# Performance work log

Measured on AMD Instinct MI355X. Metric: run time of the kernel, lower is better.

## Reference

```python
import jax, jax.numpy as jnp
import numpy as np

L, N, I, H = 512, 512, 128, 128

def setup_inputs() -> dict:
    key = jax.random.key(0)
    ks = jax.random.split(key, 6)
    inp = {
        'input': jax.random.normal(ks[0], (L, N, I), dtype=jnp.float32),
        'hc': jnp.zeros((N, 2 * H), dtype=jnp.float32),
        'is_initial': jax.random.randint(ks[1], (L, N), 0, 2, dtype=jnp.int32),
        'W_ih': jax.random.normal(ks[2], (4 * H, I), dtype=jnp.float32) * (1.0 / np.sqrt(H)),
        'W_hh': jax.random.normal(ks[3], (4 * H, H), dtype=jnp.float32) * (1.0 / np.sqrt(H)),
        'b_ih': jax.random.normal(ks[4], (4 * H,), dtype=jnp.float32) * 0.01,
        'b_hh': jax.random.normal(ks[5], (4 * H,), dtype=jnp.float32) * 0.01,
    }
    return inp

def reference(input, hc, is_initial, W_ih, W_hh, b_ih, b_hh):
    h0, c0 = jnp.split(hc, 2, axis=-1)                 # [N,H] each
    mask = 1.0 - is_initial.astype(input.dtype)        # [L,N]; 0 where episode resets

    def step(carry, xm):
        h, c = carry
        x, m = xm                                      # x:[N,I], m:[N]
        h = h * m[:, None]
        c = c * m[:, None]
        # PyTorch LSTMCell gate order: i, f, g, o
        gates = x @ W_ih.T + b_ih + h @ W_hh.T + b_hh  # [N,4H]
        i_g, f_g, g_g, o_g = jnp.split(gates, 4, axis=-1)
        i_g = jax.nn.sigmoid(i_g)
        f_g = jax.nn.sigmoid(f_g)
        g_g = jnp.tanh(g_g)
        o_g = jax.nn.sigmoid(o_g)
        c = f_g * c + i_g * g_g
        h = o_g * jnp.tanh(c)
        return (h, c), h

    (h, c), outputs = jax.lax.scan(step, (h0, c0), (input, mask))
    # final hc: cat([h,c],-1) is [N,2H]; with N==L the expand(L,-1) is a no-op
    hc_out = jnp.broadcast_to(jnp.concatenate([h, c], axis=-1), (L, 2 * H))
    return outputs, hc_out
```

## Files before the change

kernel.cpp:

```cpp
#include <hip/hip_runtime.h>
#include <hip/hip_fp16.h>
#include <stdint.h>

#define LT 512
#define NB 512
#define DI 128
#define DH 128
#define AROW 272
#define ASTR 34

typedef _Float16 f16;
typedef __attribute__((ext_vector_type(2))) _Float16 f16x2;
typedef __attribute__((ext_vector_type(8))) _Float16 f16x8;
typedef __attribute__((ext_vector_type(4))) float floatx4;

__device__ __forceinline__ uint32_t pack2(float x, float y) {
    f16x2 p;
    p.x = (_Float16)x;
    p.y = (_Float16)y;
    return __builtin_bit_cast(uint32_t, p);
}

__device__ __forceinline__ float frcp(float x) {
#if __has_builtin(__builtin_amdgcn_rcpf)
    return __builtin_amdgcn_rcpf(x);
#else
    return 1.f / x;
#endif
}

__device__ __forceinline__ float sigm(float v) {
    return frcp(1.f + __expf(-v));
}

__device__ __forceinline__ float tanh_(float v) {
    float a = fabsf(v);
    float e = __expf(-2.f * a);
    float r = (1.f - e) * frcp(1.f + e);
    return v < 0.f ? -r : r;
}

__launch_bounds__(512, 2)
__global__ void lstm_fused_mfma(const float* __restrict__ x,
                                const float* __restrict__ hc0,
                                const int*   __restrict__ isini,
                                const float* __restrict__ Wih,
                                const float* __restrict__ Whh,
                                const float* __restrict__ bih,
                                const float* __restrict__ bhh,
                                float* __restrict__ out)
{
    const int tid  = threadIdx.x;
    const int lane = tid & 63;
    const int w    = tid >> 6;
    const int l16  = lane & 15;
    const int quad = lane >> 4;
    const int n0   = blockIdx.x * 2;
    const int j    = w * 16 + l16;

    __shared__ __align__(16) f16 sh_a[2][2][AROW];
    __shared__ float sh_m[2][LT];

    for (int t = tid; t < LT; t += 512) {
        sh_m[0][t] = 1.f - (float)isini[(size_t)t * NB + n0];
        sh_m[1][t] = 1.f - (float)isini[(size_t)t * NB + n0 + 1];
    }

    f16x8 bfrag[4][8];
    float bs[4];
#pragma unroll
    for (int gs = 0; gs < 4; ++gs) {
        const int gate = gs * 128 + j;
        bs[gs] = bih[gate] + bhh[gate];
        const float4* wi = (const float4*)(Wih + (size_t)gate * DI);
        const float4* wh = (const float4*)(Whh + (size_t)gate * DH);
#pragma unroll
        for (int kc = 0; kc < 4; ++kc) {
            float4 a = wi[kc * 8 + quad * 2];
            float4 b = wi[kc * 8 + quad * 2 + 1];
            uint4 u;
            u.x = pack2(a.x, a.y); u.y = pack2(a.z, a.w);
            u.z = pack2(b.x, b.y); u.w = pack2(b.z, b.w);
            bfrag[gs][kc] = __builtin_bit_cast(f16x8, u);
        }
#pragma unroll
        for (int kc = 0; kc < 4; ++kc) {
            float4 a = wh[kc * 8 + quad * 2];
            float4 b = wh[kc * 8 + quad * 2 + 1];
            uint4 u;
            u.x = pack2(a.x, a.y); u.y = pack2(a.z, a.w);
            u.z = pack2(b.x, b.y); u.w = pack2(b.z, b.w);
            bfrag[gs][4 + kc] = __builtin_bit_cast(f16x8, u);
        }
    }

    const bool act = (quad & 1) == 0;
    const int  nr  = quad >> 1;
    const int  n   = n0 + nr;

    float cval = 0.f, hval = 0.f, mcur = 0.f;
    if (act) {
        hval = hc0[(size_t)n * (2 * DH) + j];
        cval = hc0[(size_t)n * (2 * DH) + DH + j];
        mcur = 1.f - (float)isini[n];
        sh_a[0][nr][128 + j] = (f16)(hval * mcur);
    }

    const int  sflat = w * 8 + (lane & 7);
    const int  srow  = sflat >> 5;
    const int  sf4   = sflat & 31;
    const bool sact  = (lane & 63) < 8;
    float4 xp = {0.f, 0.f, 0.f, 0.f};
    if (sact) {
        const float4* sp0 = (const float4*)(x + ((size_t)0 * NB + n0 + srow) * DI);
        float4 v = sp0[sf4];
        uint2 u2;
        u2.x = pack2(v.x, v.y); u2.y = pack2(v.z, v.w);
        *(uint2*)&sh_a[0][srow][sf4 * 4] = u2;
        const float4* sp1 = (const float4*)(x + ((size_t)1 * NB + n0 + srow) * DI);
        xp = sp1[sf4];
    }
    __syncthreads();

    const int rowsel = l16 >> 3;
    float* outp = out + (size_t)n * DH + j;

    for (int t = 0; t < LT; ++t) {
        const int buf  = t & 1;
        const int nbuf = buf ^ 1;

        const uint4* ab = (const uint4*)&sh_a[buf][0][0];
        f16x8 af[8];
#pragma unroll
        for (int kc = 0; kc < 8; ++kc)
            af[kc] = __builtin_bit_cast(f16x8, ab[rowsel * ASTR + kc * 4 + quad]);

        if (sact) {
            uint2 u2;
            u2.x = pack2(xp.x, xp.y); u2.y = pack2(xp.z, xp.w);
            *(uint2*)&sh_a[nbuf][srow][sf4 * 4] = u2;
            int t2 = (t + 2 < LT) ? (t + 2) : (LT - 1);
            const float4* sp = (const float4*)(x + ((size_t)t2 * NB + n0 + srow) * DI);
            xp = sp[sf4];
        }

        floatx4 acc[4];
#pragma unroll
        for (int gs = 0; gs < 4; ++gs) acc[gs] = (floatx4){0.f, 0.f, 0.f, 0.f};
#pragma unroll
        for (int kc = 0; kc < 8; ++kc) {
#pragma unroll
            for (int gs = 0; gs < 4; ++gs)
                acc[gs] = __builtin_amdgcn_mfma_f32_16x16x32_f16(
                    af[kc], bfrag[gs][kc], acc[gs], 0, 0, 0);
        }

        if (act) {
            float ig = acc[0][0] + bs[0];
            float fg = acc[1][0] + bs[1];
            float gg = acc[2][0] + bs[2];
            float og = acc[3][0] + bs[3];
            float cc = sigm(fg) * (mcur * cval) + sigm(ig) * tanh_(gg);
            hval = sigm(og) * tanh_(cc);
            cval = cc;
            outp[(size_t)t * (NB * DH)] = hval;
            int t1 = (t + 1 < LT) ? (t + 1) : (LT - 1);
            float mn = sh_m[nr][t1];
            sh_a[nbuf][nr][128 + j] = (f16)(hval * mn);
            mcur = mn;
        }
        __syncthreads();
    }

    if (act) {
        size_t base = (size_t)LT * NB * DH;
        out[base + (size_t)n * (2 * DH) + j]      = hval;
        out[base + (size_t)n * (2 * DH) + DH + j] = cval;
    }
}

extern "C" void kernel_launch(void* const* d_in, const int* in_sizes, int n_in,
                              void* d_out, int out_size, void* d_ws, size_t ws_size,
                              hipStream_t stream) {
    const float* x     = (const float*)d_in[0];
    const float* hc0   = (const float*)d_in[1];
    const int*   isini = (const int*)d_in[2];
    const float* Wih   = (const float*)d_in[3];
    const float* Whh   = (const float*)d_in[4];
    const float* bih   = (const float*)d_in[5];
    const float* bhh   = (const float*)d_in[6];
    float* out = (float*)d_out;

    lstm_fused_mfma<<<dim3(NB / 2), dim3(512), 0, stream>>>(
        x, hc0, isini, Wih, Whh, bih, bhh, out);
}
```

Measured before the change: 590.5 us.

## Batch input projection every 8 steps into LDS ring, halve recurrent MFMA chain

The input-to-gate projection is taken off the serial per-step critical path. Every 8 timesteps it is computed for 8 future steps at once, using a 16-row MFMA tile over staged x, and stored as packed fp16 in an LDS ring buffer. The per-step recurrent GEMM now only covers the 128-wide hidden state (4 k-chunks instead of 8), and the per-step barrier becomes a raw s_barrier after an lgkmcnt wait. The trade-offs are more LDS use, a periodic burst of extra work every 8 steps, and gate pre-activations rounded to fp16.

```diff
diff --git a/kernel.cpp b/kernel.cpp
--- a/kernel.cpp
+++ b/kernel.cpp
@@ -6,8 +6,6 @@
 #define NB 512
 #define DI 128
 #define DH 128
-#define AROW 272
-#define ASTR 34
 
 typedef _Float16 f16;
 typedef __attribute__((ext_vector_type(2))) _Float16 f16x2;
@@ -41,14 +39,14 @@
 }
 
 __launch_bounds__(512, 2)
-__global__ void lstm_fused_mfma(const float* __restrict__ x,
-                                const float* __restrict__ hc0,
-                                const int*   __restrict__ isini,
-                                const float* __restrict__ Wih,
-                                const float* __restrict__ Whh,
-                                const float* __restrict__ bih,
-                                const float* __restrict__ bhh,
-                                float* __restrict__ out)
+__global__ void lstm_fused_v2(const float* __restrict__ x,
+                              const float* __restrict__ hc0,
+                              const int*   __restrict__ isini,
+                              const float* __restrict__ Wih,
+                              const float* __restrict__ Whh,
+                              const float* __restrict__ bih,
+                              const float* __restrict__ bhh,
+                              float* __restrict__ out)
 {
     const int tid  = threadIdx.x;
     const int lane = tid & 63;
@@ -58,31 +56,22 @@
     const int n0   = blockIdx.x * 2;
     const int j    = w * 16 + l16;
 
-    __shared__ __align__(16) f16 sh_a[2][2][AROW];
+    __shared__ __align__(16) f16   sh_h[2][2][136];
+    __shared__ __align__(16) f16   xs[2][16][136];
+    __shared__ __align__(16) uint2 ring[16][2][128];
     __shared__ float sh_m[2][LT];
 
-    for (int t = tid; t < LT; t += 512) {
-        sh_m[0][t] = 1.f - (float)isini[(size_t)t * NB + n0];
-        sh_m[1][t] = 1.f - (float)isini[(size_t)t * NB + n0 + 1];
-    }
-
-    f16x8 bfrag[4][8];
+    sh_m[0][tid] = 1.f - (float)isini[(size_t)tid * NB + n0];
+    sh_m[1][tid] = 1.f - (float)isini[(size_t)tid * NB + n0 + 1];
+
+    f16x8 bH[4][4], bI[4][4];
     float bs[4];
 #pragma unroll
     for (int gs = 0; gs < 4; ++gs) {
         const int gate = gs * 128 + j;
         bs[gs] = bih[gate] + bhh[gate];
+        const float4* wh = (const float4*)(Whh + (size_t)gate * DH);
         const float4* wi = (const float4*)(Wih + (size_t)gate * DI);
-        const float4* wh = (const float4*)(Whh + (size_t)gate * DH);
-#pragma unroll
-        for (int kc = 0; kc < 4; ++kc) {
-            float4 a = wi[kc * 8 + quad * 2];
-            float4 b = wi[kc * 8 + quad * 2 + 1];
-            uint4 u;
-            u.x = pack2(a.x, a.y); u.y = pack2(a.z, a.w);
-            u.z = pack2(b.x, b.y); u.w = pack2(b.z, b.w);
-            bfrag[gs][kc] = __builtin_bit_cast(f16x8, u);
-        }
 #pragma unroll
         for (int kc = 0; kc < 4; ++kc) {
             float4 a = wh[kc * 8 + quad * 2];
@@ -90,86 +79,156 @@
             uint4 u;
             u.x = pack2(a.x, a.y); u.y = pack2(a.z, a.w);
             u.z = pack2(b.x, b.y); u.w = pack2(b.z, b.w);
-            bfrag[gs][4 + kc] = __builtin_bit_cast(f16x8, u);
-        }
-    }
+            bH[gs][kc] = __builtin_bit_cast(f16x8, u);
+            a = wi[kc * 8 + quad * 2];
+            b = wi[kc * 8 + quad * 2 + 1];
+            u.x = pack2(a.x, a.y); u.y = pack2(a.z, a.w);
+            u.z = pack2(b.x, b.y); u.w = pack2(b.z, b.w);
+            bI[gs][kc] = __builtin_bit_cast(f16x8, u);
+        }
+    }
+
+    {
+        const int m = tid >> 5, f4 = tid & 31;
+        const int d = m >> 1, nrr = m & 1;
+        const float4* sp = (const float4*)(x + ((size_t)d * NB + n0 + nrr) * DI);
+        float4 v = sp[f4];
+        uint2 u2; u2.x = pack2(v.x, v.y); u2.y = pack2(v.z, v.w);
+        *(uint2*)&xs[0][m][f4 * 4] = u2;
+    }
+    __syncthreads();
 
     const bool act = (quad & 1) == 0;
     const int  nr  = quad >> 1;
     const int  n   = n0 + nr;
-
-    float cval = 0.f, hval = 0.f, mcur = 0.f;
+    const int  rowsel = l16 >> 3;
+
+    float hval = 0.f, cval = 0.f, mcur = 0.f;
     if (act) {
         hval = hc0[(size_t)n * (2 * DH) + j];
         cval = hc0[(size_t)n * (2 * DH) + DH + j];
-        mcur = 1.f - (float)isini[n];
-        sh_a[0][nr][128 + j] = (f16)(hval * mcur);
+        mcur = sh_m[nr][0];
+        sh_h[0][nr][j] = (f16)(hval * mcur);
+    }
+
+    {
+        const uint4* xb = (const uint4*)&xs[0][0][0];
+        f16x8 axf[4];
+#pragma unroll
+        for (int kc = 0; kc < 4; ++kc)
+            axf[kc] = __builtin_bit_cast(f16x8, xb[l16 * 17 + kc * 4 + quad]);
+        floatx4 a2[4];
+#pragma unroll
+        for (int gs = 0; gs < 4; ++gs) a2[gs] = (floatx4){0.f, 0.f, 0.f, 0.f};
+#pragma unroll
+        for (int kc = 0; kc < 4; ++kc)
+#pragma unroll
+            for (int gs = 0; gs < 4; ++gs)
+                a2[gs] = __builtin_amdgcn_mfma_f32_16x16x32_f16(
+                    axf[kc], bI[gs][kc], a2[gs], 0, 0, 0);
+#pragma unroll
+        for (int r = 0; r < 4; ++r) {
+            const int m = quad * 4 + r;
+            uint2 u;
+            u.x = pack2(a2[0][r], a2[1][r]);
+            u.y = pack2(a2[2][r], a2[3][r]);
+            ring[(m >> 1) & 15][m & 1][j] = u;
+        }
+    }
+
+    {
+        const int m = tid >> 5, f4 = tid & 31;
+        const int d = m >> 1, nrr = m & 1;
+        const float4* sp = (const float4*)(x + ((size_t)(8 + d) * NB + n0 + nrr) * DI);
+        float4 v = sp[f4];
+        uint2 u2; u2.x = pack2(v.x, v.y); u2.y = pack2(v.z, v.w);
+        *(uint2*)&xs[1][m][f4 * 4] = u2;
     }
 
     const int  sflat = w * 8 + (lane & 7);
     const int  srow  = sflat >> 5;
     const int  sf4   = sflat & 31;
-    const bool sact  = (lane & 63) < 8;
-    float4 xp = {0.f, 0.f, 0.f, 0.f};
+    const bool sact  = (lane < 8);
+    float4 xp0 = {0.f, 0.f, 0.f, 0.f}, xp1 = {0.f, 0.f, 0.f, 0.f};
     if (sact) {
-        const float4* sp0 = (const float4*)(x + ((size_t)0 * NB + n0 + srow) * DI);
-        float4 v = sp0[sf4];
-        uint2 u2;
-        u2.x = pack2(v.x, v.y); u2.y = pack2(v.z, v.w);
-        *(uint2*)&sh_a[0][srow][sf4 * 4] = u2;
-        const float4* sp1 = (const float4*)(x + ((size_t)1 * NB + n0 + srow) * DI);
-        xp = sp1[sf4];
+        xp0 = ((const float4*)(x + ((size_t)16 * NB + n0 + srow) * DI))[sf4];
+        xp1 = ((const float4*)(x + ((size_t)17 * NB + n0 + srow) * DI))[sf4];
     }
     __syncthreads();
 
-    const int rowsel = l16 >> 3;
     float* outp = out + (size_t)n * DH + j;
 
     for (int t = 0; t < LT; ++t) {
-        const int buf  = t & 1;
-        const int nbuf = buf ^ 1;
-
-        const uint4* ab = (const uint4*)&sh_a[buf][0][0];
-        f16x8 af[8];
-#pragma unroll
-        for (int kc = 0; kc < 8; ++kc)
-            af[kc] = __builtin_bit_cast(f16x8, ab[rowsel * ASTR + kc * 4 + quad]);
+        if ((t & 7) == 0 && t + 8 < LT) {
+            const uint4* xb = (const uint4*)&xs[((t >> 3) + 1) & 1][0][0];
+            f16x8 axf[4];
+#pragma unroll
+            for (int kc = 0; kc < 4; ++kc)
+                axf[kc] = __builtin_bit_cast(f16x8, xb[l16 * 17 + kc * 4 + quad]);
+            floatx4 a2[4];
+#pragma unroll
+            for (int gs = 0; gs < 4; ++gs) a2[gs] = (floatx4){0.f, 0.f, 0.f, 0.f};
+#pragma unroll
+            for (int kc = 0; kc < 4; ++kc)
+#pragma unroll
+                for (int gs = 0; gs < 4; ++gs)
+                    a2[gs] = __builtin_amdgcn_mfma_f32_16x16x32_f16(
+                        axf[kc], bI[gs][kc], a2[gs], 0, 0, 0);
+            const int tb = t + 8;
+#pragma unroll
+            for (int r = 0; r < 4; ++r) {
+                const int m = quad * 4 + r;
+                uint2 u;
+                u.x = pack2(a2[0][r], a2[1][r]);
+                u.y = pack2(a2[2][r], a2[3][r]);
+                ring[(tb + (m >> 1)) & 15][m & 1][j] = u;
+            }
+        }
 
         if (sact) {
-            uint2 u2;
-            u2.x = pack2(xp.x, xp.y); u2.y = pack2(xp.z, xp.w);
-            *(uint2*)&sh_a[nbuf][srow][sf4 * 4] = u2;
-            int t2 = (t + 2 < LT) ? (t + 2) : (LT - 1);
-            const float4* sp = (const float4*)(x + ((size_t)t2 * NB + n0 + srow) * DI);
-            xp = sp[sf4];
-        }
-
+            uint2 u2; u2.x = pack2(xp0.x, xp0.y); u2.y = pack2(xp0.z, xp0.w);
+            *(uint2*)&xs[(t >> 3) & 1][2 * (t & 7) + srow][sf4 * 4] = u2;
+            xp0 = xp1;
+            const int tl = t + 18;
+            if (tl < LT)
+                xp1 = ((const float4*)(x + ((size_t)tl * NB + n0 + srow) * DI))[sf4];
+        }
+
+        const uint4* hb = (const uint4*)&sh_h[t & 1][0][0];
+        f16x8 af[4];
+#pragma unroll
+        for (int kc = 0; kc < 4; ++kc)
+            af[kc] = __builtin_bit_cast(f16x8, hb[rowsel * 17 + kc * 4 + quad]);
         floatx4 acc[4];
 #pragma unroll
         for (int gs = 0; gs < 4; ++gs) acc[gs] = (floatx4){0.f, 0.f, 0.f, 0.f};
 #pragma unroll
-        for (int kc = 0; kc < 8; ++kc) {
+        for (int kc = 0; kc < 4; ++kc)
 #pragma unroll
             for (int gs = 0; gs < 4; ++gs)
                 acc[gs] = __builtin_amdgcn_mfma_f32_16x16x32_f16(
-                    af[kc], bfrag[gs][kc], acc[gs], 0, 0, 0);
-        }
+                    af[kc], bH[gs][kc], acc[gs], 0, 0, 0);
 
         if (act) {
-            float ig = acc[0][0] + bs[0];
-            float fg = acc[1][0] + bs[1];
-            float gg = acc[2][0] + bs[2];
-            float og = acc[3][0] + bs[3];
+            const uint2 rv = ring[t & 15][nr][j];
+            const f16x2 p01 = __builtin_bit_cast(f16x2, rv.x);
+            const f16x2 p23 = __builtin_bit_cast(f16x2, rv.y);
+            float ig = (float)p01.x + bs[0] + acc[0][0];
+            float fg = (float)p01.y + bs[1] + acc[1][0];
+            float gg = (float)p23.x + bs[2] + acc[2][0];
+            float og = (float)p23.y + bs[3] + acc[3][0];
             float cc = sigm(fg) * (mcur * cval) + sigm(ig) * tanh_(gg);
             hval = sigm(og) * tanh_(cc);
             cval = cc;
             outp[(size_t)t * (NB * DH)] = hval;
-            int t1 = (t + 1 < LT) ? (t + 1) : (LT - 1);
-            float mn = sh_m[nr][t1];
-            sh_a[nbuf][nr][128 + j] = (f16)(hval * mn);
+            const int t1 = (t + 1 < LT) ? (t + 1) : (LT - 1);
+            const float mn = sh_m[nr][t1];
+            sh_h[(t + 1) & 1][nr][j] = (f16)(hval * mn);
             mcur = mn;
         }
-        __syncthreads();
+
+        asm volatile("s_waitcnt lgkmcnt(0)" ::: "memory");
+        __builtin_amdgcn_s_barrier();
     }
 
     if (act) {
@@ -191,6 +250,6 @@
     const float* bhh   = (const float*)d_in[6];
     float* out = (float*)d_out;
 
-    lstm_fused_mfma<<<dim3(NB / 2), dim3(512), 0, stream>>>(
+    lstm_fused_v2<<<dim3(NB / 2), dim3(512), 0, stream>>>(
         x, hc0, isini, Wih, Whh, bih, bhh, out);
 }
```

Measured after the change: 595.5 us. About the same (+0.8%).
